# Kernel optimization log

Hardware: AMD Instinct MI355X
Metric: run time of the kernel (lower is better)

The kernel has to match this reference:

```python
import jax, jax.numpy as jnp
import numpy as np

RADIUS = 0.05      # outer ball-query radius
MIN_RADIUS = 0.02  # inner exclusion radius


def setup_inputs() -> dict:
    key = jax.random.key(0)
    k1, k2 = jax.random.split(key)
    # raw layout is [B, C, N, 1] as consumed by forward's squeeze(-1).permute(0,2,1)
    xyz = jax.random.uniform(k1, (4, 3, 4096, 1), dtype=jnp.float32)      # coords in unit cube
    points = jax.random.normal(k2, (4, 64, 4096, 1), dtype=jnp.float32)   # per-point features
    return {"xyz": xyz, "points": points}


def _pairwise_sqdist(x):
    # x: [B, N, 3] -> [B, N, N] squared euclidean distances
    sq = jnp.sum(x * x, axis=-1)  # [B, N]
    return sq[:, :, None] + sq[:, None, :] - 2.0 * jnp.einsum('bnc,bmc->bnm', x, x)


def reference(xyz, points):
    # [B, C, N, 1] -> [B, N, C]
    _xyz = jnp.transpose(xyz[..., 0], (0, 2, 1))       # [B, N, 3]
    _points = jnp.transpose(points[..., 0], (0, 2, 1))  # [B, N, D]
    B, N, C = _xyz.shape

    # downsample_query_ball: ball-query neighbor counts in annulus (min_radius, radius),
    # keep the N//2 densest points
    d2 = _pairwise_sqdist(_xyz)                              # [B, N, N]
    nbr_cnt = jnp.sum(((d2 < RADIUS ** 2) & (d2 > MIN_RADIUS ** 2)).astype(jnp.int32), axis=-1)
    _, idx = jax.lax.top_k(nbr_cnt, N // 2)                  # [B, N//2]

    # index_points: gather along the point axis
    new_xyz = jnp.take_along_axis(_xyz, idx[..., None], axis=1)        # [B, N//2, 3]
    new_points = jnp.take_along_axis(_points, idx[..., None], axis=1)  # [B, N//2, D]
    return new_xyz, new_points
```

## Files before the change

### kernel.cpp

```cpp
#include <hip/hip_runtime.h>


#pragma clang fp contract(off)

#define BN 4
#define NPTS 4096
#define ND 64
#define KSEL 2048
#define R2 0.0025f
#define M2 0.0004f
#define NCELL 4096
#define CS_STRIDE 4100

typedef unsigned int u32;
typedef unsigned short u16;

#define OFF_SORTED 0
#define OFF_SIDX   262144
#define OFF_CS     294912
#define OFF_PART   360512

__global__ __launch_bounds__(1024) void bin_kernel(
        const float* __restrict__ xyz, float4* __restrict__ sorted,
        u16* __restrict__ sidx, u32* __restrict__ cellstart) {
    __shared__ u32 hist[NCELL];
    __shared__ u32 wtot[16];
    const int b = blockIdx.x;
    const float* base = xyz + (size_t)b * 3 * NPTS;
    const int tid = threadIdx.x;
    for (int k = tid; k < NCELL; k += 1024) hist[k] = 0u;
    __syncthreads();

    u32 crk[4];
    #pragma unroll
    for (int k = 0; k < 4; ++k) {
        const int i = tid + k * 1024;
        float x = base[i], y = base[NPTS + i], z = base[2 * NPTS + i];
        int c = (int)(x * 16.0f) | ((int)(y * 16.0f) << 4)
                                 | ((int)(z * 16.0f) << 8);
        u32 r = atomicAdd(&hist[c], 1u);
        crk[k] = ((u32)c << 16) | r;
    }
    __syncthreads();

    u32 v4[4], sum = 0;
    #pragma unroll
    for (int k = 0; k < 4; ++k) { v4[k] = hist[tid * 4 + k]; sum += v4[k]; }
    const int lane = tid & 63, w = tid >> 6;
    u32 incl = sum;
    #pragma unroll
    for (int d = 1; d < 64; d <<= 1) {
        u32 t = __shfl_up(incl, d, 64);
        if (lane >= d) incl += t;
    }
    if (lane == 63) wtot[w] = incl;
    __syncthreads();
    u32 woff = 0;
    #pragma unroll
    for (int ww = 0; ww < 16; ++ww) woff += (ww < w) ? wtot[ww] : 0u;
    u32 run = woff + incl - sum;
    #pragma unroll
    for (int k = 0; k < 4; ++k) { u32 h = v4[k]; hist[tid * 4 + k] = run; run += h; }
    __syncthreads();

    u32* csb = cellstart + b * CS_STRIDE;
    #pragma unroll
    for (int k = 0; k < 4; ++k) {
        const int i = tid + k * 1024;
        float x = base[i], y = base[NPTS + i], z = base[2 * NPTS + i];
        float sq = __fadd_rn(__fadd_rn(__fmul_rn(x, x), __fmul_rn(y, y)),
                             __fmul_rn(z, z));
        u32 c = crk[k] >> 16, r = crk[k] & 0xFFFFu;
        u32 pos = hist[c] + r;
        sorted[((size_t)b << 12) + pos] = make_float4(x, y, z, sq);
        sidx[((size_t)b << 12) + pos]   = (u16)i;
    }
    for (int k = tid; k < NCELL; k += 1024) csb[k] = hist[k];
    if (tid == 0) csb[NCELL] = NPTS;
}

__global__ __launch_bounds__(256) void count_grid_kernel(
        const float4* __restrict__ sorted, const u32* __restrict__ cellstart,
        u16* __restrict__ part3) {
    const int g  = blockIdx.x * 256 + threadIdx.x;
    const int b  = g / (3 * NPTS);
    const int rg = g - b * 3 * NPTS;
    const int dz = rg >> 12;
    const int p  = rg & (NPTS - 1);

    const float4* sb = sorted + ((size_t)b << 12);
    const float4 v = sb[p];
    const int cx = (int)(v.x * 16.0f);
    const int cy = (int)(v.y * 16.0f);
    const int cz = (int)(v.z * 16.0f);
    const int zz = cz + dz - 1;

    const int      m2i1  = __float_as_int(M2) + 1;
    const unsigned range = (unsigned)(__float_as_int(R2) - __float_as_int(M2)) - 1u;

    u32 cnt = 0;
    if ((unsigned)zz < 16u) {
        const u32* cs = cellstart + b * CS_STRIDE + (zz << 8);
        const int x0  = (cx > 0)  ? cx - 1 : 0;
        const int x1e = ((cx < 15) ? cx + 1 : 15) + 1;
        const int y0  = (cy > 0)  ? cy - 1 : 0;
        const int y1  = (cy < 15) ? cy + 1 : 15;
        for (int y = y0; y <= y1; ++y) {
            u32 s = cs[(y << 4) + x0];
            u32 e = cs[(y << 4) + x1e];
            for (u32 q = s; q < e; ++q) {
                float4 u = sb[q];
                float dot = __fadd_rn(__fadd_rn(__fmul_rn(v.x, u.x),
                                                __fmul_rn(v.y, u.y)),
                                      __fmul_rn(v.z, u.z));
                float spw = __fadd_rn(v.w, u.w);
                float d2  = __builtin_fmaf(dot, -2.0f, spw);
                cnt += ((unsigned)(__float_as_int(d2) - m2i1) < range) ? 1u : 0u;
            }
        }
    }
    part3[((size_t)((b << 12) | p) << 2) + dz] = (u16)cnt;
}

__global__ __launch_bounds__(256) void rank_gather_kernel(
        const float* __restrict__ xyz, const float* __restrict__ points,
        const u16* __restrict__ part3, const u16* __restrict__ sidx,
        float* __restrict__ out) {
    __shared__ union {
        alignas(16) int skey[NPTS];
        float sfeat[ND][68];
    } sh;
    __shared__ int spr[4][64];
    __shared__ int srank[64];
    const int b     = blockIdx.x >> 6;
    const int tbase = (blockIdx.x & 63) * 64;
    const int tid   = threadIdx.x;

    {
        const uint4* pq = (const uint4*)(part3 + ((size_t)b << 12) * 4);
        const u32*   sx = (const u32*)(sidx + ((size_t)b << 12));
        #pragma unroll
        for (int r = 0; r < 8; ++r) {
            const int gp = r * 256 + tid;
            uint4 q = pq[gp];
            u32  od = sx[gp];
            u32 c0 = (q.x & 0xFFFFu) + (q.x >> 16) + (q.y & 0xFFFFu);
            u32 c1 = (q.z & 0xFFFFu) + (q.z >> 16) + (q.w & 0xFFFFu);
            int o0 = (int)(od & 0xFFFFu), o1 = (int)(od >> 16);
            sh.skey[o0] = (int)(c0 << 12) | (NPTS - 1 - o0);
            sh.skey[o1] = (int)(c1 << 12) | (NPTS - 1 - o1);
        }
    }
    __syncthreads();

    {
        const int pi = tid & 63;
        const int q  = tid >> 6;
        const int ki = sh.skey[tbase + pi];
        const int4* sk4 = (const int4*)sh.skey;
        int r = 0;
        #pragma unroll 8
        for (int jj = q * 256; jj < q * 256 + 256; ++jj) {
            int4 v = sk4[jj];
            r += (v.x > ki) ? 1 : 0;
            r += (v.y > ki) ? 1 : 0;
            r += (v.z > ki) ? 1 : 0;
            r += (v.w > ki) ? 1 : 0;
        }
        spr[q][pi] = r;
    }
    __syncthreads();

    if (tid < 64) {
        const int rank = spr[0][tid] + spr[1][tid] + spr[2][tid] + spr[3][tid];
        srank[tid] = rank;
        const int i = tbase + tid;
        if (rank < KSEL) {
            const float* xb = xyz + (size_t)b * 3 * NPTS;
            float* o = out + ((size_t)b * KSEL + rank) * 3;
            o[0] = xb[i]; o[1] = xb[NPTS + i]; o[2] = xb[2 * NPTS + i];
        }
    }
    __syncthreads();

    {
        const int ii = tid & 63;
        const int q  = tid >> 6;
        #pragma unroll
        for (int r16 = 0; r16 < 16; ++r16) {
            const int c = q + 4 * r16;
            sh.sfeat[c][ii] = points[((size_t)b * ND + c) * NPTS + tbase + ii];
        }
    }
    __syncthreads();

    {
        const int pt = tid >> 2;
        const int c4 = tid & 3;
        const int rank = srank[pt];
        if (rank < KSEL) {
            float* orow = out + (size_t)BN * KSEL * 3 +
                          ((size_t)b * KSEL + rank) * ND;
            #pragma unroll
            for (int u4 = 0; u4 < 4; ++u4) {
                const int c0 = u4 * 16 + c4 * 4;
                float4 v = make_float4(sh.sfeat[c0 + 0][pt],
                                       sh.sfeat[c0 + 1][pt],
                                       sh.sfeat[c0 + 2][pt],
                                       sh.sfeat[c0 + 3][pt]);
                *(float4*)(orow + c0) = v;
            }
        }
    }
}

extern "C" void kernel_launch(void* const* d_in, const int* in_sizes, int n_in,
                              void* d_out, int out_size, void* d_ws, size_t ws_size,
                              hipStream_t stream) {
    const float* xyz    = (const float*)d_in[0];
    const float* points = (const float*)d_in[1];
    float* out = (float*)d_out;
    char*  ws  = (char*)d_ws;

    float4* sorted   = (float4*)(ws + OFF_SORTED);
    u16*    sidx     = (u16*)  (ws + OFF_SIDX);
    u32*    cellstart= (u32*)  (ws + OFF_CS);
    u16*    part3    = (u16*)  (ws + OFF_PART);

    bin_kernel       <<<BN, 1024, 0, stream>>>(xyz, sorted, sidx, cellstart);
    count_grid_kernel<<<BN * 3 * NPTS / 256, 256, 0, stream>>>(sorted, cellstart, part3);
    rank_gather_kernel<<<BN * 64, 256, 0, stream>>>(xyz, points, part3, sidx, out);
}
```

Measured before the change: 78.43 us.

## Fuse z-slab count reduction into count kernel and prefetch features early

The count kernel now puts the three z-slab partial counts of each point into one block, sums them in shared memory, and writes a finished sort key (count plus inverted original index) in sorted order. The rank kernel then scatters those keys straight into shared memory by original index, without decoding partial counts and the index map. The rank kernel also issues its feature and xyz global loads into registers before the rank phase, so load latency overlaps the comparison loop. The bin kernel keeps coordinates in registers instead of reloading them, and writes cell starts during the scan. The cost is more registers in the rank kernel and a block-level sync in the count kernel.

```diff
diff --git a/kernel.cpp b/kernel.cpp
--- a/kernel.cpp
+++ b/kernel.cpp
@@ -18,7 +18,7 @@
 #define OFF_SORTED 0
 #define OFF_SIDX   262144
 #define OFF_CS     294912
-#define OFF_PART   360512
+#define OFF_KEYS   360512
 
 __global__ __launch_bounds__(1024) void bin_kernel(
         const float* __restrict__ xyz, float4* __restrict__ sorted,
@@ -31,6 +31,7 @@
     for (int k = tid; k < NCELL; k += 1024) hist[k] = 0u;
     __syncthreads();
 
+    float xk[4], yk[4], zk[4];
     u32 crk[4];
     #pragma unroll
     for (int k = 0; k < 4; ++k) {
@@ -40,6 +41,7 @@
                                  | ((int)(z * 16.0f) << 8);
         u32 r = atomicAdd(&hist[c], 1u);
         crk[k] = ((u32)c << 16) | r;
+        xk[k] = x; yk[k] = y; zk[k] = z;
     }
     __syncthreads();
 
@@ -58,42 +60,47 @@
     u32 woff = 0;
     #pragma unroll
     for (int ww = 0; ww < 16; ++ww) woff += (ww < w) ? wtot[ww] : 0u;
+    u32* csb = cellstart + b * CS_STRIDE;
     u32 run = woff + incl - sum;
     #pragma unroll
-    for (int k = 0; k < 4; ++k) { u32 h = v4[k]; hist[tid * 4 + k] = run; run += h; }
-    __syncthreads();
-
-    u32* csb = cellstart + b * CS_STRIDE;
-    #pragma unroll
     for (int k = 0; k < 4; ++k) {
-        const int i = tid + k * 1024;
-        float x = base[i], y = base[NPTS + i], z = base[2 * NPTS + i];
+        u32 h = v4[k];
+        hist[tid * 4 + k] = run;
+        csb[tid * 4 + k]  = run;
+        run += h;
+    }
+    if (tid == 0) csb[NCELL] = NPTS;
+    __syncthreads();
+
+    #pragma unroll
+    for (int k = 0; k < 4; ++k) {
+        float x = xk[k], y = yk[k], z = zk[k];
         float sq = __fadd_rn(__fadd_rn(__fmul_rn(x, x), __fmul_rn(y, y)),
                              __fmul_rn(z, z));
         u32 c = crk[k] >> 16, r = crk[k] & 0xFFFFu;
         u32 pos = hist[c] + r;
         sorted[((size_t)b << 12) + pos] = make_float4(x, y, z, sq);
-        sidx[((size_t)b << 12) + pos]   = (u16)i;
-    }
-    for (int k = tid; k < NCELL; k += 1024) csb[k] = hist[k];
-    if (tid == 0) csb[NCELL] = NPTS;
-}
-
-__global__ __launch_bounds__(256) void count_grid_kernel(
+        sidx[((size_t)b << 12) + pos]   = (u16)(tid + k * 1024);
+    }
+}
+
+__global__ __launch_bounds__(192) void count_key_kernel(
         const float4* __restrict__ sorted, const u32* __restrict__ cellstart,
-        u16* __restrict__ part3) {
-    const int g  = blockIdx.x * 256 + threadIdx.x;
-    const int b  = g / (3 * NPTS);
-    const int rg = g - b * 3 * NPTS;
-    const int dz = rg >> 12;
-    const int p  = rg & (NPTS - 1);
+        const u16* __restrict__ sidx, u32* __restrict__ keys) {
+    __shared__ u32 spart[3][64];
+    const int tid  = threadIdx.x;
+    const int lane = tid & 63;
+    const int w    = tid >> 6;
+    const int gp   = blockIdx.x * 64;
+    const int b    = gp >> 12;
+    const int p    = (gp & (NPTS - 1)) + lane;
 
     const float4* sb = sorted + ((size_t)b << 12);
     const float4 v = sb[p];
     const int cx = (int)(v.x * 16.0f);
     const int cy = (int)(v.y * 16.0f);
     const int cz = (int)(v.z * 16.0f);
-    const int zz = cz + dz - 1;
+    const int zz = cz + w - 1;
 
     const int      m2i1  = __float_as_int(M2) + 1;
     const unsigned range = (unsigned)(__float_as_int(R2) - __float_as_int(M2)) - 1u;
@@ -119,13 +126,18 @@
             }
         }
     }
-    part3[((size_t)((b << 12) | p) << 2) + dz] = (u16)cnt;
+    spart[w][lane] = cnt;
+    __syncthreads();
+    if (tid < 64) {
+        u32 c = spart[0][lane] + spart[1][lane] + spart[2][lane];
+        const int orig = sidx[((size_t)b << 12) + p];
+        keys[((size_t)b << 12) + p] = (c << 12) | (u32)(NPTS - 1 - orig);
+    }
 }
 
 __global__ __launch_bounds__(256) void rank_gather_kernel(
         const float* __restrict__ xyz, const float* __restrict__ points,
-        const u16* __restrict__ part3, const u16* __restrict__ sidx,
-        float* __restrict__ out) {
+        const u32* __restrict__ keys, float* __restrict__ out) {
     __shared__ union {
         alignas(16) int skey[NPTS];
         float sfeat[ND][68];
@@ -135,28 +147,37 @@
     const int b     = blockIdx.x >> 6;
     const int tbase = (blockIdx.x & 63) * 64;
     const int tid   = threadIdx.x;
-
-    {
-        const uint4* pq = (const uint4*)(part3 + ((size_t)b << 12) * 4);
-        const u32*   sx = (const u32*)(sidx + ((size_t)b << 12));
+    const int ii    = tid & 63;
+    const int q     = tid >> 6;
+
+    float fv[16];
+    {
+        const float* pb = points + ((size_t)b * ND + q) * NPTS + tbase + ii;
         #pragma unroll
-        for (int r = 0; r < 8; ++r) {
-            const int gp = r * 256 + tid;
-            uint4 q = pq[gp];
-            u32  od = sx[gp];
-            u32 c0 = (q.x & 0xFFFFu) + (q.x >> 16) + (q.y & 0xFFFFu);
-            u32 c1 = (q.z & 0xFFFFu) + (q.z >> 16) + (q.w & 0xFFFFu);
-            int o0 = (int)(od & 0xFFFFu), o1 = (int)(od >> 16);
-            sh.skey[o0] = (int)(c0 << 12) | (NPTS - 1 - o0);
-            sh.skey[o1] = (int)(c1 << 12) | (NPTS - 1 - o1);
-        }
-    }
-    __syncthreads();
-
-    {
-        const int pi = tid & 63;
-        const int q  = tid >> 6;
-        const int ki = sh.skey[tbase + pi];
+        for (int r16 = 0; r16 < 16; ++r16)
+            fv[r16] = pb[(size_t)(4 * r16) * NPTS];
+    }
+    float x3[3];
+    if (tid < 64) {
+        const float* xb = xyz + (size_t)b * 3 * NPTS + tbase + tid;
+        x3[0] = xb[0]; x3[1] = xb[NPTS]; x3[2] = xb[2 * NPTS];
+    }
+
+    {
+        const int4* kq = (const int4*)(keys + ((size_t)b << 12));
+        #pragma unroll
+        for (int r = 0; r < 4; ++r) {
+            int4 v = kq[r * 256 + tid];
+            sh.skey[NPTS - 1 - (v.x & 0xFFF)] = v.x;
+            sh.skey[NPTS - 1 - (v.y & 0xFFF)] = v.y;
+            sh.skey[NPTS - 1 - (v.z & 0xFFF)] = v.z;
+            sh.skey[NPTS - 1 - (v.w & 0xFFF)] = v.w;
+        }
+    }
+    __syncthreads();
+
+    {
+        const int ki = sh.skey[tbase + ii];
         const int4* sk4 = (const int4*)sh.skey;
         int r = 0;
         #pragma unroll 8
@@ -167,30 +188,24 @@
             r += (v.z > ki) ? 1 : 0;
             r += (v.w > ki) ? 1 : 0;
         }
-        spr[q][pi] = r;
+        spr[q][ii] = r;
     }
     __syncthreads();
 
     if (tid < 64) {
         const int rank = spr[0][tid] + spr[1][tid] + spr[2][tid] + spr[3][tid];
         srank[tid] = rank;
-        const int i = tbase + tid;
         if (rank < KSEL) {
-            const float* xb = xyz + (size_t)b * 3 * NPTS;
             float* o = out + ((size_t)b * KSEL + rank) * 3;
-            o[0] = xb[i]; o[1] = xb[NPTS + i]; o[2] = xb[2 * NPTS + i];
-        }
-    }
-    __syncthreads();
-
-    {
-        const int ii = tid & 63;
-        const int q  = tid >> 6;
+            o[0] = x3[0]; o[1] = x3[1]; o[2] = x3[2];
+        }
+    }
+    __syncthreads();
+
+    {
         #pragma unroll
-        for (int r16 = 0; r16 < 16; ++r16) {
-            const int c = q + 4 * r16;
-            sh.sfeat[c][ii] = points[((size_t)b * ND + c) * NPTS + tbase + ii];
-        }
+        for (int r16 = 0; r16 < 16; ++r16)
+            sh.sfeat[q + 4 * r16][ii] = fv[r16];
     }
     __syncthreads();
 
@@ -222,12 +237,12 @@
     float* out = (float*)d_out;
     char*  ws  = (char*)d_ws;
 
-    float4* sorted   = (float4*)(ws + OFF_SORTED);
-    u16*    sidx     = (u16*)  (ws + OFF_SIDX);
-    u32*    cellstart= (u32*)  (ws + OFF_CS);
-    u16*    part3    = (u16*)  (ws + OFF_PART);
+    float4* sorted    = (float4*)(ws + OFF_SORTED);
+    u16*    sidx      = (u16*)  (ws + OFF_SIDX);
+    u32*    cellstart = (u32*)  (ws + OFF_CS);
+    u32*    keys      = (u32*)  (ws + OFF_KEYS);
 
     bin_kernel       <<<BN, 1024, 0, stream>>>(xyz, sorted, sidx, cellstart);
-    count_grid_kernel<<<BN * 3 * NPTS / 256, 256, 0, stream>>>(sorted, cellstart, part3);
-    rank_gather_kernel<<<BN * 64, 256, 0, stream>>>(xyz, points, part3, sidx, out);
-}
+    count_key_kernel <<<BN * NPTS / 64, 192, 0, stream>>>(sorted, cellstart, sidx, keys);
+    rank_gather_kernel<<<BN * 64, 256, 0, stream>>>(xyz, points, keys, out);
+}
```

Result: no change. 78.06 us (-0.5%).
